# Kernel tuning notes

Measured on AMD Instinct MI355X. Metric: run time of the kernel, lower is better.

Reference implementation:

```python
import jax, jax.numpy as jnp
import numpy as np

N = 100000      # nodes
E = 1600000     # edges
IN_DIM = 256
HID = 64
NCLS = 32


def setup_inputs() -> dict:
    key = jax.random.key(0)
    ks = jax.random.split(key, 7)
    features = jax.random.normal(ks[0], (N, IN_DIM), dtype=jnp.float32)
    hidden_prev = jax.random.normal(ks[1], (N, HID), dtype=jnp.float32)
    adj_indices = jax.random.randint(ks[2], (2, E), 0, N, dtype=jnp.int32)
    # torch.rand init, scaled by 0.1 to keep activations numerically sane
    W0 = jax.random.uniform(ks[3], (IN_DIM, HID), dtype=jnp.float32) * 0.1
    W1 = jax.random.uniform(ks[4], (HID, HID), dtype=jnp.float32) * 0.1
    W2 = jax.random.uniform(ks[5], (HID, NCLS), dtype=jnp.float32) * 0.1
    att_w = jax.random.uniform(ks[6], (2 * HID, 1), dtype=jnp.float32) * 0.1
    return {"features": features, "hidden_prev": hidden_prev,
            "adj_indices": adj_indices, "W0": W0, "W1": W1, "W2": W2,
            "att_w": att_w}


def _edge_softmax(scores, rows, n):
    # sparse softmax over dim=1 of an NxN COO: normalize per source row
    m = jax.ops.segment_max(scores, rows, num_segments=n)
    ex = jnp.exp(scores - m[rows])
    s = jax.ops.segment_sum(ex, rows, num_segments=n)
    return ex / s[rows]


def _compute_attention(hfeat, adj_indices, att_w):
    src, dst = adj_indices[0], adj_indices[1]
    h = hfeat.shape[1]
    # cat(f_src, f_dst) @ att_w == f_src @ w_a + f_dst @ w_b ; project per-node
    proj_a = hfeat @ att_w[:h, 0]   # [N]
    proj_b = hfeat @ att_w[h:, 0]   # [N]
    scores = jax.nn.leaky_relu(proj_a[src] + proj_b[dst])  # [E]
    return _edge_softmax(scores, src, hfeat.shape[0])


def _spmm(att_vals, adj_indices, x):
    # out[i] = sum_{(i,j) in E} att * x[j]
    src, dst = adj_indices[0], adj_indices[1]
    return jax.ops.segment_sum(att_vals[:, None] * x[dst], src,
                               num_segments=x.shape[0])


def reference(features, hidden_prev, adj_indices, W0, W1, W2, att_w):
    att = _compute_attention(hidden_prev, adj_indices, att_w)  # [E]
    h = features
    for W in (W0, W1, W2):
        h = jax.nn.elu(_spmm(att, adj_indices, h @ W))
    return jax.nn.log_softmax(h, axis=1)
```

## Files before the change

kernel.cpp:

```cpp
#include <hip/hip_runtime.h>
#include <math.h>

#define HIDN 64
#define NCLS_K 32
#define INDIM 256
#define BSHIFT 7
#define MAXBUCK 1024
#define BUCK_CAP 4096
#define DSTBITS 17
#define DSTMASK ((1 << DSTBITS) - 1)

typedef unsigned int uint;
typedef unsigned short ushort;
typedef __attribute__((ext_vector_type(8))) short short8v;
typedef __attribute__((ext_vector_type(4))) float f32x4;

__device__ inline float bflo(uint u) { return __uint_as_float(u << 16); }
__device__ inline float bfhi(uint u) { return __uint_as_float(u & 0xFFFF0000u); }
__device__ inline ushort f2bf(float f) {
  uint u = __float_as_uint(f);
  return (ushort)((u + 0x7FFFu + ((u >> 16) & 1u)) >> 16);
}
__device__ inline float bf2f(ushort h) { return __uint_as_float(((uint)h) << 16); }

__global__ __launch_bounds__(256) void proj_kernel(const float* __restrict__ hid,
    const float* __restrict__ attw, float* __restrict__ pa, float* __restrict__ pb, int n) {
  int wid  = (blockIdx.x * blockDim.x + threadIdx.x) >> 6;
  int lane = threadIdx.x & 63;
  if (wid >= n) return;
  float v = hid[(size_t)wid * HIDN + lane];
  float a = v * attw[lane];
  float b = v * attw[HIDN + lane];
  #pragma unroll
  for (int off = 32; off >= 1; off >>= 1) {
    a += __shfl_xor(a, off, 64);
    b += __shfl_xor(b, off, 64);
  }
  if (lane == 0) { pa[wid] = a; pb[wid] = b; }
}

__global__ __launch_bounds__(256) void hist_kernel(const int* __restrict__ src,
    int* __restrict__ bcnt, int e, int nb) {
  __shared__ int h[MAXBUCK];
  for (int j = threadIdx.x; j < MAXBUCK; j += 256) h[j] = 0;
  __syncthreads();
  for (int i = blockIdx.x * 256 + threadIdx.x; i < e; i += gridDim.x * 256)
    atomicAdd(&h[src[i] >> BSHIFT], 1);
  __syncthreads();
  for (int j = threadIdx.x; j < nb; j += 256)
    if (h[j]) atomicAdd(&bcnt[j], h[j]);
}

__global__ __launch_bounds__(1024) void scan_buckets(const int* __restrict__ bcnt,
    int* __restrict__ bbase, int* __restrict__ rowp, int nb, int n, int e) {
  __shared__ int sm[1024];
  int tid = threadIdx.x;
  int v = (tid < nb) ? bcnt[tid] : 0;
  sm[tid] = v;
  __syncthreads();
  for (int off = 1; off < 1024; off <<= 1) {
    int t = (tid >= off) ? sm[tid - off] : 0;
    __syncthreads();
    sm[tid] += t;
    __syncthreads();
  }
  if (tid < nb) bbase[tid] = sm[tid] - v;
  if (tid == 0) { bbase[nb] = e; rowp[n] = e; }
}

__global__ __launch_bounds__(256) void scatter_pairs(const int* __restrict__ src,
    const int* __restrict__ dst, const int* __restrict__ bbase,
    int* __restrict__ bcur, int* __restrict__ pairs, int e, int nb) {
  __shared__ int h[MAXBUCK];
  int nper = (e + gridDim.x - 1) / gridDim.x;
  int lo = blockIdx.x * nper;
  int hi = min(e, lo + nper);
  for (int j = threadIdx.x; j < nb; j += 256) h[j] = 0;
  __syncthreads();
  for (int i = lo + threadIdx.x; i < hi; i += 256)
    atomicAdd(&h[src[i] >> BSHIFT], 1);
  __syncthreads();
  for (int j = threadIdx.x; j < nb; j += 256) {
    int c = h[j];
    h[j] = c ? (bbase[j] + atomicAdd(&bcur[j], c)) : 0;
  }
  __syncthreads();
  for (int i = lo + threadIdx.x; i < hi; i += 256) {
    int s = src[i];
    int pos = atomicAdd(&h[s >> BSHIFT], 1);
    pairs[pos] = ((s & 127) << DSTBITS) | dst[i];
  }
}

__global__ __launch_bounds__(256) void build_csr(const int* __restrict__ pairs,
    const int* __restrict__ bbase, int* __restrict__ rowp,
    int* __restrict__ dstc, int n) {
  __shared__ int hist[128];
  __shared__ int cur[128];
  __shared__ int ord[BUCK_CAP];
  int b = blockIdx.x;
  int tid = threadIdx.x;
  int base = bbase[b];
  int m = bbase[b + 1] - base;
  if (tid < 128) hist[tid] = 0;
  __syncthreads();
  for (int i = tid; i < m; i += 256)
    atomicAdd(&hist[pairs[base + i] >> DSTBITS], 1);
  __syncthreads();
  int own = (tid < 128) ? hist[tid] : 0;
  for (int off = 1; off < 128; off <<= 1) {
    int t = (tid < 128 && tid >= off) ? hist[tid - off] : 0;
    __syncthreads();
    if (tid < 128) hist[tid] += t;
    __syncthreads();
  }
  if (tid < 128) {
    int excl = hist[tid] - own;
    cur[tid] = excl;
    int s = (b << BSHIFT) + tid;
    if (s < n) rowp[s] = base + excl;
  }
  __syncthreads();
  for (int i = tid; i < m; i += 256) {
    int key = pairs[base + i];
    int pos = atomicAdd(&cur[key >> DSTBITS], 1);
    ord[pos] = key;
  }
  __syncthreads();
  for (int i = tid; i < m; i += 256) dstc[base + i] = ord[i];
}

__device__ inline int wave_sort64(int key, int lane) {
  #pragma unroll
  for (int k = 2; k <= 64; k <<= 1) {
    #pragma unroll
    for (int j = k >> 1; j > 0; j >>= 1) {
      int p = __shfl_xor(key, j, 64);
      bool up    = ((lane & k) == 0);
      bool lower = ((lane & j) == 0);
      int mn = min(key, p), mx = max(key, p);
      key = (lower == up) ? mn : mx;
    }
  }
  return key;
}

__global__ __launch_bounds__(256) void att_softmax(const float* __restrict__ pa,
    const float* __restrict__ pb, int* __restrict__ dstc,
    const int* __restrict__ rowp, ushort* __restrict__ attb, int n) {
  int wid  = (blockIdx.x * blockDim.x + threadIdx.x) >> 6;
  int lane = threadIdx.x & 63;
  if (wid >= n) return;
  int start = rowp[wid], end = rowp[wid + 1];
  int c = end - start;
  if (c <= 0) return;
  float pai = pa[wid];
  if (c <= 64) {
    int e = start + lane;
    int key = (lane < c) ? dstc[e] : 0x7FFFFFFF;
    key = wave_sort64(key, lane);
    float s = -3.0e38f;
    if (lane < c) {
      dstc[e] = key;
      float v = pai + pb[key & DSTMASK];
      s = v > 0.f ? v : 0.01f * v;
    }
    float m = s;
    #pragma unroll
    for (int off = 32; off >= 1; off >>= 1) m = fmaxf(m, __shfl_xor(m, off, 64));
    float ex = (lane < c) ? expf(s - m) : 0.f;
    float sum = ex;
    #pragma unroll
    for (int off = 32; off >= 1; off >>= 1) sum += __shfl_xor(sum, off, 64);
    if (lane < c) attb[e] = f2bf(ex / sum);
    return;
  }
  float m = -3.0e38f;
  for (int base = start; base < end; base += 64) {
    int e = base + lane;
    int key = (e < end) ? dstc[e] : 0x7FFFFFFF;
    key = wave_sort64(key, lane);
    float s = -3.0e38f;
    if (e < end) {
      dstc[e] = key;
      float v = pai + pb[key & DSTMASK];
      s = v > 0.f ? v : 0.01f * v;
      attb[e] = f2bf(s);
    }
    m = fmaxf(m, s);
  }
  #pragma unroll
  for (int off = 32; off >= 1; off >>= 1) m = fmaxf(m, __shfl_xor(m, off, 64));
  float sum = 0.f;
  for (int base = start; base < end; base += 64) {
    int e = base + lane;
    float ex = 0.f;
    if (e < end) { ex = expf(bf2f(attb[e]) - m); attb[e] = f2bf(ex); }
    sum += ex;
  }
  #pragma unroll
  for (int off = 32; off >= 1; off >>= 1) sum += __shfl_xor(sum, off, 64);
  float inv = 1.f / sum;
  for (int base = start; base < end; base += 64) {
    int e = base + lane;
    if (e < end) attb[e] = f2bf(bf2f(attb[e]) * inv);
  }
}

template <int K, int TJ>
__global__ __launch_bounds__(256) void gemm_mfma(const float* __restrict__ A,
    const float* __restrict__ W, ushort* __restrict__ Xb, int n) {
  constexpr int KP = K + 8;
  constexpr int NCB = TJ / 16;
  __shared__ ushort Wt[TJ][KP];
  const int tid = threadIdx.x;
  for (int idx = tid; idx < K * TJ; idx += 256) {
    int k = idx / TJ, j = idx % TJ;
    Wt[j][k] = f2bf(W[idx]);
  }
  __syncthreads();
  const int wv   = blockIdx.x * 4 + (tid >> 6);
  const int row0 = wv * 16;
  if (row0 >= n) return;
  const int lane = tid & 63;
  const int r    = lane & 15;
  const int kg   = lane >> 4;
  const int rowA = min(row0 + r, n - 1);
  const float* ap = A + (size_t)rowA * K + kg * 8;

  f32x4 acc[NCB];
  #pragma unroll
  for (int c = 0; c < NCB; ++c) acc[c] = (f32x4)(0.f);

  #pragma unroll
  for (int ks = 0; ks < K / 32; ++ks) {
    float4 a0 = *reinterpret_cast<const float4*>(ap + ks * 32);
    float4 a1 = *reinterpret_cast<const float4*>(ap + ks * 32 + 4);
    union { short8v v; ushort u[8]; } af;
    af.u[0] = f2bf(a0.x); af.u[1] = f2bf(a0.y);
    af.u[2] = f2bf(a0.z); af.u[3] = f2bf(a0.w);
    af.u[4] = f2bf(a1.x); af.u[5] = f2bf(a1.y);
    af.u[6] = f2bf(a1.z); af.u[7] = f2bf(a1.w);
    #pragma unroll
    for (int c = 0; c < NCB; ++c) {
      short8v bf = *reinterpret_cast<const short8v*>(&Wt[c * 16 + r][ks * 32 + kg * 8]);
      acc[c] = __builtin_amdgcn_mfma_f32_16x16x32_bf16(af.v, bf, acc[c], 0, 0, 0);
    }
  }
  #pragma unroll
  for (int c = 0; c < NCB; ++c) {
    #pragma unroll
    for (int i = 0; i < 4; ++i) {
      int rowS = row0 + kg * 4 + i;
      if (rowS < n) Xb[(size_t)rowS * TJ + c * 16 + r] = f2bf(acc[c][i]);
    }
  }
}

template <int TJ, bool FINAL>
__global__ __launch_bounds__(256) void spmm_mfma(const ushort* __restrict__ Xb,
    const ushort* __restrict__ attb, const int* __restrict__ dstc,
    const int* __restrict__ rowp, float* __restrict__ out, int n) {
  constexpr int NCB = TJ / 16;
  const int tid  = threadIdx.x;
  const int g    = blockIdx.x * 4 + (tid >> 6);
  const int row0 = g * 16;
  if (row0 >= n) return;
  const int lane = tid & 63;
  const int r    = lane & 15;
  const int kg   = lane >> 4;
  const int start = rowp[row0];
  const int end   = rowp[min(row0 + 16, n)];

  f32x4 acc[NCB];
  #pragma unroll
  for (int c = 0; c < NCB; ++c) acc[c] = (f32x4)(0.f);

  for (int base = start; base < end; base += 32) {
    int sbase = base + 8 * kg;
    union { short8v v; ushort u[8]; } af;
    int dv[8];
    #pragma unroll
    for (int j = 0; j < 8; ++j) {
      int e = sbase + j;
      bool valid = e < end;
      int idx = valid ? e : (end - 1);
      int v = dstc[idx];
      ushort a = attb[idx];
      int rid = (v >> DSTBITS) & 15;
      af.u[j] = (valid && rid == r) ? a : (ushort)0;
      dv[j] = v & DSTMASK;
    }
    #pragma unroll
    for (int c = 0; c < NCB; ++c) {
      union { short8v v; ushort u[8]; } bf;
      #pragma unroll
      for (int j = 0; j < 8; ++j)
        bf.u[j] = Xb[(size_t)dv[j] * TJ + c * 16 + r];
      acc[c] = __builtin_amdgcn_mfma_f32_16x16x32_bf16(af.v, bf.v, acc[c], 0, 0, 0);
    }
  }
  #pragma unroll
  for (int c = 0; c < NCB; ++c)
    #pragma unroll
    for (int i = 0; i < 4; ++i)
      acc[c][i] = acc[c][i] > 0.f ? acc[c][i] : (expf(acc[c][i]) - 1.f);
  if (!FINAL) {
    #pragma unroll
    for (int c = 0; c < NCB; ++c)
      #pragma unroll
      for (int i = 0; i < 4; ++i) {
        int rowS = row0 + kg * 4 + i;
        if (rowS < n) out[(size_t)rowS * TJ + c * 16 + r] = acc[c][i];
      }
  } else {
    #pragma unroll
    for (int i = 0; i < 4; ++i) {
      float m = acc[0][i];
      #pragma unroll
      for (int c = 1; c < NCB; ++c) m = fmaxf(m, acc[c][i]);
      #pragma unroll
      for (int off = 1; off < 16; off <<= 1) m = fmaxf(m, __shfl_xor(m, off));
      float s = 0.f;
      #pragma unroll
      for (int c = 0; c < NCB; ++c) s += expf(acc[c][i] - m);
      #pragma unroll
      for (int off = 1; off < 16; off <<= 1) s += __shfl_xor(s, off);
      float lg = m + logf(s);
      int rowS = row0 + kg * 4 + i;
      if (rowS < n) {
        #pragma unroll
        for (int c = 0; c < NCB; ++c)
          out[(size_t)rowS * TJ + c * 16 + r] = acc[c][i] - lg;
      }
    }
  }
}

extern "C" void kernel_launch(void* const* d_in, const int* in_sizes, int n_in,
                              void* d_out, int out_size, void* d_ws, size_t ws_size,
                              hipStream_t stream) {
  const float* features = (const float*)d_in[0];
  const float* hidden   = (const float*)d_in[1];
  const int*   adj      = (const int*)d_in[2];
  const float* W0       = (const float*)d_in[3];
  const float* W1       = (const float*)d_in[4];
  const float* W2       = (const float*)d_in[5];
  const float* attw     = (const float*)d_in[6];
  float* out = (float*)d_out;

  const int N = in_sizes[1] / HIDN;
  const int E = in_sizes[2] / 2;
  const int* src = adj;
  const int* dst = adj + E;
  const int NBUCK = (N + 127) >> BSHIFT;
  const int NB2   = ((NBUCK + 15) / 16) * 16;

  int*   rowp  = (int*)d_ws;
  int*   bbase = rowp + (N + 16);
  int*   bcnt  = bbase + (NB2 + 16);
  int*   bcur  = bcnt + NB2;
  int*   dstc  = bcur + NB2;
  ushort* attb = (ushort*)(dstc + E);
  float* Xf    = (float*)(attb) + (E / 2 + 16);
  float* H     = Xf + (size_t)N * HIDN;
  ushort* Xb   = (ushort*)Xf;
  int*   pairs = (int*)Xf;
  float* pa    = H;
  float* pb    = H + N;

  (void)hipMemsetAsync(bcnt, 0, (size_t)2 * NB2 * sizeof(int), stream);

  dim3 blk(256);
  const int gridWave = (N + 3) / 4;
  const int gridG16  = ((N + 15) / 16 + 3) / 4;

  proj_kernel<<<gridWave, blk, 0, stream>>>(hidden, attw, pa, pb, N);
  hist_kernel<<<512, blk, 0, stream>>>(src, bcnt, E, NBUCK);
  scan_buckets<<<1, 1024, 0, stream>>>(bcnt, bbase, rowp, NBUCK, N, E);
  scatter_pairs<<<128, blk, 0, stream>>>(src, dst, bbase, bcur, pairs, E, NBUCK);
  build_csr<<<NBUCK, blk, 0, stream>>>(pairs, bbase, rowp, dstc, N);
  att_softmax<<<gridWave, blk, 0, stream>>>(pa, pb, dstc, rowp, attb, N);

  gemm_mfma<INDIM, HIDN><<<gridG16, blk, 0, stream>>>(features, W0, Xb, N);
  spmm_mfma<HIDN, false><<<gridG16, blk, 0, stream>>>(Xb, attb, dstc, rowp, H, N);
  gemm_mfma<HIDN, HIDN><<<gridG16, blk, 0, stream>>>(H, W1, Xb, N);
  spmm_mfma<HIDN, false><<<gridG16, blk, 0, stream>>>(Xb, attb, dstc, rowp, H, N);
  gemm_mfma<HIDN, NCLS_K><<<gridG16, blk, 0, stream>>>(H, W2, Xb, N);
  spmm_mfma<NCLS_K, true><<<gridG16, blk, 0, stream>>>(Xb, attb, dstc, rowp, out, N);
}
```

Measured before the change: 325.1 us.

## Replace atomic bucket offsets with per-block histogram matrix and column scan

The counting sort that builds the CSR now stores a per-block bucket histogram matrix (512 blocks) and runs a column-wise exclusive scan, which gives each block fixed per-bucket write offsets. The scatter kernel no longer re-histograms its chunk and no longer needs global atomics on bucket cursors. The memset goes away and the scatter grid grows from 128 to 512 blocks. In exchange there is one more kernel launch and an NBUCK×512 int matrix in the workspace.

Result: faster. 310.9 us (-4.4%).

```diff
diff --git a/kernel.cpp b/kernel.cpp
--- a/kernel.cpp
+++ b/kernel.cpp
@@ -9,14 +9,13 @@
 #define BUCK_CAP 4096
 #define DSTBITS 17
 #define DSTMASK ((1 << DSTBITS) - 1)
+#define SCB 512
 
 typedef unsigned int uint;
 typedef unsigned short ushort;
 typedef __attribute__((ext_vector_type(8))) short short8v;
 typedef __attribute__((ext_vector_type(4))) float f32x4;
 
-__device__ inline float bflo(uint u) { return __uint_as_float(u << 16); }
-__device__ inline float bfhi(uint u) { return __uint_as_float(u & 0xFFFF0000u); }
 __device__ inline ushort f2bf(float f) {
   uint u = __float_as_uint(f);
   return (ushort)((u + 0x7FFFu + ((u >> 16) & 1u)) >> 16);
@@ -39,16 +38,41 @@
   if (lane == 0) { pa[wid] = a; pb[wid] = b; }
 }
 
-__global__ __launch_bounds__(256) void hist_kernel(const int* __restrict__ src,
-    int* __restrict__ bcnt, int e, int nb) {
+__global__ __launch_bounds__(256) void hist2(const int* __restrict__ src,
+    int* __restrict__ hmatT, int e, int nb, int nper) {
   __shared__ int h[MAXBUCK];
-  for (int j = threadIdx.x; j < MAXBUCK; j += 256) h[j] = 0;
-  __syncthreads();
-  for (int i = blockIdx.x * 256 + threadIdx.x; i < e; i += gridDim.x * 256)
+  int lo = blockIdx.x * nper;
+  int hi = min(e, lo + nper);
+  for (int j = threadIdx.x; j < nb; j += 256) h[j] = 0;
+  __syncthreads();
+  for (int i = lo + threadIdx.x; i < hi; i += 256)
     atomicAdd(&h[src[i] >> BSHIFT], 1);
   __syncthreads();
   for (int j = threadIdx.x; j < nb; j += 256)
-    if (h[j]) atomicAdd(&bcnt[j], h[j]);
+    hmatT[(size_t)j * SCB + blockIdx.x] = h[j];
+}
+
+__global__ __launch_bounds__(256) void col_scan(int* __restrict__ hmatT,
+    int* __restrict__ bcnt, int nb) {
+  constexpr int PER = SCB / 64;
+  int wv = blockIdx.x * 4 + (threadIdx.x >> 6);
+  if (wv >= nb) return;
+  int lane = threadIdx.x & 63;
+  int* col = hmatT + (size_t)wv * SCB + lane * PER;
+  int v[PER];
+  int s = 0;
+  #pragma unroll
+  for (int q = 0; q < PER; ++q) { v[q] = col[q]; s += v[q]; }
+  int x = s;
+  #pragma unroll
+  for (int off = 1; off < 64; off <<= 1) {
+    int t = __shfl_up(x, off, 64);
+    if (lane >= off) x += t;
+  }
+  int pre = x - s;
+  #pragma unroll
+  for (int q = 0; q < PER; ++q) { int t = v[q]; col[q] = pre; pre += t; }
+  if (lane == 63) bcnt[wv] = pre;
 }
 
 __global__ __launch_bounds__(1024) void scan_buckets(const int* __restrict__ bcnt,
@@ -68,22 +92,14 @@
   if (tid == 0) { bbase[nb] = e; rowp[n] = e; }
 }
 
-__global__ __launch_bounds__(256) void scatter_pairs(const int* __restrict__ src,
-    const int* __restrict__ dst, const int* __restrict__ bbase,
-    int* __restrict__ bcur, int* __restrict__ pairs, int e, int nb) {
+__global__ __launch_bounds__(256) void scatter2(const int* __restrict__ src,
+    const int* __restrict__ dst, const int* __restrict__ hmatT,
+    const int* __restrict__ bbase, int* __restrict__ pairs, int e, int nb, int nper) {
   __shared__ int h[MAXBUCK];
-  int nper = (e + gridDim.x - 1) / gridDim.x;
   int lo = blockIdx.x * nper;
   int hi = min(e, lo + nper);
-  for (int j = threadIdx.x; j < nb; j += 256) h[j] = 0;
-  __syncthreads();
-  for (int i = lo + threadIdx.x; i < hi; i += 256)
-    atomicAdd(&h[src[i] >> BSHIFT], 1);
-  __syncthreads();
-  for (int j = threadIdx.x; j < nb; j += 256) {
-    int c = h[j];
-    h[j] = c ? (bbase[j] + atomicAdd(&bcur[j], c)) : 0;
-  }
+  for (int j = threadIdx.x; j < nb; j += 256)
+    h[j] = bbase[j] + hmatT[(size_t)j * SCB + blockIdx.x];
   __syncthreads();
   for (int i = lo + threadIdx.x; i < hi; i += 256) {
     int s = src[i];
@@ -355,12 +371,13 @@
   const int* dst = adj + E;
   const int NBUCK = (N + 127) >> BSHIFT;
   const int NB2   = ((NBUCK + 15) / 16) * 16;
+  const int nper  = (E + SCB - 1) / SCB;
 
   int*   rowp  = (int*)d_ws;
   int*   bbase = rowp + (N + 16);
   int*   bcnt  = bbase + (NB2 + 16);
-  int*   bcur  = bcnt + NB2;
-  int*   dstc  = bcur + NB2;
+  int*   hmatT = bcnt + NB2;
+  int*   dstc  = hmatT + (size_t)NBUCK * SCB;
   ushort* attb = (ushort*)(dstc + E);
   float* Xf    = (float*)(attb) + (E / 2 + 16);
   float* H     = Xf + (size_t)N * HIDN;
@@ -369,16 +386,15 @@
   float* pa    = H;
   float* pb    = H + N;
 
-  (void)hipMemsetAsync(bcnt, 0, (size_t)2 * NB2 * sizeof(int), stream);
-
   dim3 blk(256);
   const int gridWave = (N + 3) / 4;
   const int gridG16  = ((N + 15) / 16 + 3) / 4;
 
   proj_kernel<<<gridWave, blk, 0, stream>>>(hidden, attw, pa, pb, N);
-  hist_kernel<<<512, blk, 0, stream>>>(src, bcnt, E, NBUCK);
+  hist2<<<SCB, blk, 0, stream>>>(src, hmatT, E, NBUCK, nper);
+  col_scan<<<(NBUCK + 3) / 4, blk, 0, stream>>>(hmatT, bcnt, NBUCK);
   scan_buckets<<<1, 1024, 0, stream>>>(bcnt, bbase, rowp, NBUCK, N, E);
-  scatter_pairs<<<128, blk, 0, stream>>>(src, dst, bbase, bcur, pairs, E, NBUCK);
+  scatter2<<<SCB, blk, 0, stream>>>(src, dst, hmatT, bbase, pairs, E, NBUCK, nper);
   build_csr<<<NBUCK, blk, 0, stream>>>(pairs, bbase, rowp, dstc, N);
   att_softmax<<<gridWave, blk, 0, stream>>>(pa, pb, dstc, rowp, attb, N);
 
```
